# Optimization experiments

Measured on AMD Instinct MI355X. Metric: run time of the kernel, lower is better.

## Reference

```python
import jax, jax.numpy as jnp
import numpy as np

NF, NS, GP = 5, 27, 4


def conv2d(x, w, b):
    y = jax.lax.conv_general_dilated(x, w, (1, 1), 'SAME',
                                     dimension_numbers=('NCHW', 'OIHW', 'NCHW'))
    return y + b[None, :, None, None]


def trilinear_sample(frames, tc, yc, xc):
    # frames: [b, nf, h, w]; tc/yc/xc: [b, NS, h, w] absolute (t, y, x) coords
    b, nf, h, w = frames.shape
    tc = jnp.clip(tc, 0.0, nf - 1.0)
    yc = jnp.clip(yc, 0.0, h - 1.0)
    xc = jnp.clip(xc, 0.0, w - 1.0)
    t0 = jnp.floor(tc); y0 = jnp.floor(yc); x0 = jnp.floor(xc)
    wt = tc - t0; wy = yc - y0; wx = xc - x0
    t0i = t0.astype(jnp.int32); y0i = y0.astype(jnp.int32); x0i = x0.astype(jnp.int32)
    t1i = jnp.minimum(t0i + 1, nf - 1)
    y1i = jnp.minimum(y0i + 1, h - 1)
    x1i = jnp.minimum(x0i + 1, w - 1)
    flat = frames.reshape(b, -1)

    def g(ti, yi, xi):
        idx = (ti * h + yi) * w + xi  # [b, NS, h, w]
        return jnp.take_along_axis(flat, idx.reshape(b, -1), axis=1).reshape(idx.shape)

    c000 = g(t0i, y0i, x0i); c001 = g(t0i, y0i, x1i)
    c010 = g(t0i, y1i, x0i); c011 = g(t0i, y1i, x1i)
    c100 = g(t1i, y0i, x0i); c101 = g(t1i, y0i, x1i)
    c110 = g(t1i, y1i, x0i); c111 = g(t1i, y1i, x1i)
    c00 = c000 * (1 - wx) + c001 * wx
    c01 = c010 * (1 - wx) + c011 * wx
    c10 = c100 * (1 - wx) + c101 * wx
    c11 = c110 * (1 - wx) + c111 * wx
    c0 = c00 * (1 - wy) + c01 * wy
    c1 = c10 * (1 - wy) + c11 * wy
    return c0 * (1 - wt) + c1 * wt


def samp(frames, offset):
    # offset: [b, NS*3, h, w] -> per-sample (dt, dy, dx)
    b, nf, h, w = frames.shape
    off = offset.reshape(b, NS, 3, h, w)
    grid = np.stack(np.meshgrid(np.arange(-1, 2), np.arange(-1, 2), np.arange(-1, 2),
                                indexing='ij'), -1).reshape(NS, 3).astype(np.float32)
    bt = jnp.asarray(grid[:, 0] + (NF - 1) // 2)[None, :, None, None]
    by = jnp.asarray(grid[:, 1])[None, :, None, None]
    bx = jnp.asarray(grid[:, 2])[None, :, None, None]
    yy = jnp.arange(h, dtype=frames.dtype)[None, None, :, None]
    xx = jnp.arange(w, dtype=frames.dtype)[None, None, None, :]
    tc = off[:, :, 0] + bt
    yc = off[:, :, 1] + by + yy
    xc = off[:, :, 2] + bx + xx
    return trilinear_sample(frames, tc, yc, xc)  # [b, NS, h, w]


def reference(frames, ow1, ob1, ow2, ob2, ow3, ob3, ww1, wb1, ww2, wb2, ww3, wb3):
    b, c, h, w = frames.shape
    # OffsetNet: two relu convs -> feat (128 ch), head -> offsets (NS*3 ch)
    f1 = jax.nn.relu(conv2d(frames, ow1, ob1))
    feat = jax.nn.relu(conv2d(f1, ow2, ob2))
    offset = conv2d(feat, ow3, ob3)
    samples = samp(frames, offset)  # [b, 27, h, w]
    cat = jnp.concatenate([frames, feat, samples], axis=1)  # [b, 160, h, w]
    # WeightsNet: three conv+relu
    wgt = jax.nn.relu(conv2d(cat, ww1, wb1))
    wgt = jax.nn.relu(conv2d(wgt, ww2, wb2))
    wgt = jax.nn.relu(conv2d(wgt, ww3, wb3))  # [b, 27, h, w]
    npg = NS // GP  # 6 -> only first GP*npg=24 samples used (torch.split + range(gp))
    s = samples[:, :GP * npg].reshape(b, GP, npg, h, w)
    wg = wgt[:, :GP * npg].reshape(b, GP, npg, h, w)
    gp_pred = GP * jnp.sum(s * wg, axis=2)  # [b, 4, h, w]
    avg = jnp.sum(gp_pred, axis=1, keepdims=True) / NS
    return gp_pred, avg


def setup_inputs() -> dict:
    key = jax.random.key(0)
    ks = jax.random.split(key, 8)
    B, H, W = 4, 512, 512

    def he(k, shape):
        fan_in = shape[1] * shape[2] * shape[3]
        return jax.random.normal(k, shape, jnp.float32) * np.sqrt(2.0 / fan_in)

    return {
        'frames': jax.random.uniform(ks[0], (B, NF, H, W), jnp.float32),
        'ow1': he(ks[1], (64, NF, 3, 3)), 'ob1': jnp.zeros((64,), jnp.float32),
        'ow2': he(ks[2], (128, 64, 3, 3)), 'ob2': jnp.zeros((128,), jnp.float32),
        'ow3': he(ks[3], (NS * 3, 128, 3, 3)) * 0.1, 'ob3': jnp.zeros((NS * 3,), jnp.float32),
        'ww1': he(ks[4], (64, NF + 128 + NS, 3, 3)), 'wb1': jnp.zeros((64,), jnp.float32),
        'ww2': he(ks[5], (64, 64, 3, 3)), 'wb2': jnp.zeros((64,), jnp.float32),
        'ww3': he(ks[6], (NS, 64, 3, 3)), 'wb3': jnp.zeros((NS,), jnp.float32),
    }
```

## Files before the change

### kernel.cpp

```cpp
#include <hip/hip_runtime.h>

#define HH 512
#define WW 512
#define HWP (HH * WW)

typedef unsigned short bf16_t;
typedef short bf16x8 __attribute__((ext_vector_type(8)));
typedef float f32x4 __attribute__((ext_vector_type(4)));
typedef unsigned short us4 __attribute__((ext_vector_type(4)));
typedef unsigned short us8 __attribute__((ext_vector_type(8)));

__device__ __forceinline__ float bf2f(bf16_t h) {
    union { unsigned int u; float f; } v; v.u = ((unsigned int)h) << 16; return v.f;
}
__device__ __forceinline__ bf16_t f2bf(float f) {
    union { float f; unsigned int u; } v; v.f = f;
    unsigned int r = (v.u + 0x7FFFu + ((v.u >> 16) & 1u)) >> 16;
    return (bf16_t)r;
}
__device__ __forceinline__ bf16x8 as_bf(us8 v) {
    union { us8 a; bf16x8 b; } u; u.a = v; return u.b;
}
__device__ __forceinline__ void gload16(const void* g, void* l) {
    __builtin_amdgcn_global_load_lds(
        (const __attribute__((address_space(1))) void*)g,
        (__attribute__((address_space(3))) void*)l, 16, 0, 0);
}

__global__ __launch_bounds__(256) void wprep_all(
    const float* __restrict__ w1, const float* __restrict__ w2,
    const float* __restrict__ w3, const float* __restrict__ w4,
    const float* __restrict__ w5, const float* __restrict__ w6,
    bf16_t* __restrict__ dst)
{
    int i = blockIdx.x * 256 + threadIdx.x;
    if (i >= 350720) return;
    if (i >= 350208) { dst[i] = 0; return; }
    const float* w; int Cout, Cin, COTF, KS, perm, base;
    if (i < 18432)       { w = w1; base = 0;      Cout = 64;  Cin = 5;   COTF = 4; KS = 1; perm = 0; }
    else if (i < 92160)  { w = w2; base = 18432;  Cout = 128; Cin = 64;  COTF = 8; KS = 2; perm = 0; }
    else if (i < 202752) { w = w3; base = 92160;  Cout = 81;  Cin = 128; COTF = 6; KS = 4; perm = 0; }
    else if (i < 294912) { w = w4; base = 202752; Cout = 64;  Cin = 160; COTF = 4; KS = 5; perm = 1; }
    else if (i < 331776) { w = w5; base = 294912; Cout = 64;  Cin = 64;  COTF = 4; KS = 2; perm = 0; }
    else                 { w = w6; base = 331776; Cout = 27;  Cin = 64;  COTF = 2; KS = 2; perm = 0; }
    int r = i - base;
    int j = r & 7;
    int lane = (r >> 3) & 63;
    int cot = (r >> 9) % COTF;
    int rest = r / (512 * COTF);
    int ks = rest % KS, tap = rest / KS;
    int col = lane & 15, hi = lane >> 4;
    int co = cot * 16 + col;
    int ci = ks * 32 + hi * 8 + j;
    float v = 0.f;
    if (co < Cout && ci < Cin) {
        int rci = ci;
        if (perm) rci = (ci < 128) ? ci + 5 : (ci < 133 ? ci - 128 : ci);
        v = w[((size_t)co * Cin + rci) * 9 + tap];
    }
    dst[i] = f2bf(v);
}

template<int COT, int KS, int ZX>
__global__ __launch_bounds__(256, 2) void tconv(
    const bf16_t* __restrict__ in, size_t inImgStride,
    const bf16_t* __restrict__ wt, const float* __restrict__ bias,
    bf16_t* __restrict__ out, size_t outImgStride,
    int COTF, int Cout, int relu, const bf16_t* __restrict__ zp,
    int cinCh, const bf16_t* __restrict__ catp,
    float* __restrict__ fuseOut, int img0)
{
    __shared__ us8 buf[2][1584];
    const int tid = threadIdx.x;
    const int wave = tid >> 6, lane = tid & 63;
    const int col = lane & 15, hi = lane >> 4;
    const int img = blockIdx.y >> 7;
    const int yb0 = (blockIdx.y & 127) * 4;
    const int xb = (ZX ? (blockIdx.x >> 1) : blockIdx.x) * 64;
    const int czbase = (ZX ? (blockIdx.x & 1) : blockIdx.z) * COT;
    const size_t slab = (size_t)HH * WW * 32;

    in += (size_t)img * inImgStride;
    out += (size_t)img * outImgStride;

    int gofs[7];
    bool ok[7];
#pragma unroll
    for (int k = 0; k < 7; ++k) {
        int u = tid + k * 256;
        if (u >= 1584) u = 1583;
        int row = (unsigned)u / 264u;
        int rem = u - row * 264;
        int px = rem >> 2, cs = rem & 3;
        int c = (cs - (px >> 1)) & 3;
        int yin = yb0 - 1 + row;
        int gx = xb - 1 + px;
        ok[k] = ((unsigned)yin < (unsigned)HH) && ((unsigned)gx < (unsigned)WW)
                && (c < cinCh);
        gofs[k] = ok[k] ? (int)(((size_t)yin * WW + gx) * 32 + c * 8) : 0;
    }

    auto STAGE = [&](int nb, int ks) {
#pragma unroll
        for (int k = 0; k < 7; ++k) {
            if (k == 6 && tid >= 48) continue;
            const bf16_t* g = ok[k] ? in + (size_t)ks * slab + gofs[k] : zp;
            gload16(g, (void*)&buf[nb][k * 256 + wave * 64]);
        }
    };

    f32x4 acc[4][COT] = {};
    bf16x8 a[9][COT];

    auto ALOAD = [&](int ks) {
#pragma unroll
        for (int t = 0; t < 9; ++t) {
#pragma unroll
            for (int c = 0; c < COT; ++c)
                a[t][c] = *(const bf16x8*)(wt
                    + (((size_t)t * KS + ks) * COTF + czbase + c) * 512 + lane * 8);
        }
    };

    auto COMPUTE = [&](int cb) {
#pragma unroll
        for (int dx = 0; dx < 3; ++dx) {
            const int X = wave * 16 + col + dx;
            const int ubase = X * 4 + ((hi + (X >> 1)) & 3);
            bf16x8 b[6];
#pragma unroll
            for (int br = 0; br < 6; ++br)
                b[br] = as_bf(buf[cb][br * 264 + ubase]);
#pragma unroll
            for (int dy = 0; dy < 3; ++dy) {
#pragma unroll
                for (int c = 0; c < COT; ++c) {
#pragma unroll
                    for (int r = 0; r < 4; ++r)
                        acc[r][c] = __builtin_amdgcn_mfma_f32_16x16x32_bf16(
                            a[dy * 3 + dx][c], b[r + dy], acc[r][c], 0, 0, 0);
                }
            }
        }
    };

    STAGE(0, 0);
    for (int ks = 0; ks < KS; ++ks) {
        ALOAD(ks);
        __builtin_amdgcn_sched_barrier(0);
        if (ks + 1 < KS) {
            STAGE((ks + 1) & 1, ks + 1);
            __builtin_amdgcn_sched_barrier(0);
            asm volatile("s_waitcnt vmcnt(7)" ::: "memory");
        } else {
            asm volatile("s_waitcnt vmcnt(0)" ::: "memory");
        }
        __builtin_amdgcn_sched_barrier(0);
        __builtin_amdgcn_s_barrier();
        __builtin_amdgcn_sched_barrier(0);
        COMPUTE(ks & 1);
        __builtin_amdgcn_s_barrier();
        __builtin_amdgcn_sched_barrier(0);
    }

    const int x = xb + wave * 16 + col;

    if (fuseOut) {
        int gimg = img0 + img;
        const bf16_t* catim = catp + (size_t)img * inImgStride;
#pragma unroll
        for (int r = 0; r < 4; ++r) {
            int y = yb0 + r;
            const bf16_t* cp = catim + ((size_t)y * WW + x) * 32;
            float p[4] = {0.f, 0.f, 0.f, 0.f};
#pragma unroll
            for (int c = 0; c < COT; ++c) {
                int chb = (czbase + c) * 16 + hi * 4;
#pragma unroll
                for (int j = 0; j < 4; ++j) {
                    int ch = chb + j;
                    if (ch < 24) {
                        float wv = fmaxf(acc[r][c][j] + bias[ch], 0.f);
                        p[ch / 6] += wv * bf2f(cp[5 + ch]);
                    }
                }
            }
#pragma unroll
            for (int g = 0; g < 4; ++g) {
                p[g] += __shfl_xor(p[g], 16);
                p[g] += __shfl_xor(p[g], 32);
            }
            if (hi == 0) {
                size_t pix = (size_t)y * WW + x;
                float tot = 0.f;
#pragma unroll
                for (int g = 0; g < 4; ++g) {
                    float gp = 4.f * p[g];
                    fuseOut[((size_t)gimg * 4 + g) * HWP + pix] = gp;
                    tot += gp;
                }
                fuseOut[(size_t)16 * HWP + (size_t)gimg * HWP + pix] = tot / 27.f;
            }
        }
        return;
    }

#pragma unroll
    for (int c = 0; c < COT; ++c) {
        int chbase = (czbase + c) * 16 + hi * 4;
        int slice = chbase >> 5, rem = chbase & 31;
        float bv[4];
#pragma unroll
        for (int j = 0; j < 4; ++j) {
            int co = chbase + j;
            bv[j] = (co < Cout) ? bias[co] : 0.f;
        }
#pragma unroll
        for (int r = 0; r < 4; ++r) {
            int y = yb0 + r;
            us4 o;
#pragma unroll
            for (int j = 0; j < 4; ++j) {
                float v = acc[r][c][j] + bv[j];
                if (relu) v = fmaxf(v, 0.f);
                o[j] = f2bf(v);
            }
            *(us4*)(out + (((size_t)slice * HH + y) * WW + x) * 32 + rem) = o;
        }
    }
}

__global__ __launch_bounds__(256) void tr_fr32(
    const float* __restrict__ fr0, int img0,
    bf16_t* __restrict__ dst0, size_t stride)
{
    int img = blockIdx.y;
    int i = blockIdx.x * 256 + threadIdx.x;
    const float* fr = fr0 + (size_t)(img0 + img) * 5 * HWP;
    bf16_t* dst = dst0 + (size_t)img * stride;
    us8 v0 = {};
#pragma unroll
    for (int c = 0; c < 5; ++c) v0[c] = f2bf(fr[(size_t)c * HWP + i]);
    *(us8*)(dst + (size_t)i * 32) = v0;
}

__global__ __launch_bounds__(256, 4) void sample27f(
    const float* __restrict__ fr0, int img0,
    const bf16_t* __restrict__ of0, size_t stride,
    bf16_t* __restrict__ cat0)
{
    int img = blockIdx.y;
    int i = blockIdx.x * 256 + threadIdx.x;
    int y = i >> 9, x = i & 511;
    const float* f = fr0 + (size_t)(img0 + img) * 5 * HWP;
    const bf16_t* off = of0 + (size_t)img * stride;
    bf16_t* cat = cat0 + (size_t)img * stride;

    us8 ov[12];
#pragma unroll
    for (int sl = 0; sl < 3; ++sl)
#pragma unroll
        for (int c = 0; c < 4; ++c)
            ov[sl * 4 + c] = *(const us8*)(off
                + (((size_t)sl * HH + y) * WW + x) * 32 + c * 8);

    us8 outv[4];
#pragma unroll
    for (int c = 0; c < 5; ++c)
        outv[0][c] = f2bf(f[(size_t)c * HWP + i]);

#pragma unroll
    for (int s = 0; s < 27; ++s) {
        float dt  = bf2f((bf16_t)ov[(3 * s) >> 3][(3 * s) & 7]);
        float dyo = bf2f((bf16_t)ov[(3 * s + 1) >> 3][(3 * s + 1) & 7]);
        float dxo = bf2f((bf16_t)ov[(3 * s + 2) >> 3][(3 * s + 2) & 7]);
        float tc = dt + (float)(s / 9 + 1);
        float yc = dyo + (float)((s / 3) % 3 - 1) + (float)y;
        float xc = dxo + (float)(s % 3 - 1) + (float)x;
        tc = fminf(fmaxf(tc, 0.f), 4.f);
        yc = fminf(fmaxf(yc, 0.f), 511.f);
        xc = fminf(fmaxf(xc, 0.f), 511.f);
        float t0f = floorf(tc), y0f = floorf(yc), x0f = floorf(xc);
        float wt = tc - t0f, wy = yc - y0f, wx = xc - x0f;
        int t0 = (int)t0f, y0 = (int)y0f, x0 = (int)x0f;
        int t1 = min(t0 + 1, 4), y1 = min(y0 + 1, 511), x1 = min(x0 + 1, 511);
        float c000 = f[((size_t)t0 * HH + y0) * WW + x0];
        float c001 = f[((size_t)t0 * HH + y0) * WW + x1];
        float c010 = f[((size_t)t0 * HH + y1) * WW + x0];
        float c011 = f[((size_t)t0 * HH + y1) * WW + x1];
        float c100 = f[((size_t)t1 * HH + y0) * WW + x0];
        float c101 = f[((size_t)t1 * HH + y0) * WW + x1];
        float c110 = f[((size_t)t1 * HH + y1) * WW + x0];
        float c111 = f[((size_t)t1 * HH + y1) * WW + x1];
        float c00 = c000 * (1.f - wx) + c001 * wx;
        float c01 = c010 * (1.f - wx) + c011 * wx;
        float c10 = c100 * (1.f - wx) + c101 * wx;
        float c11 = c110 * (1.f - wx) + c111 * wx;
        float c0 = c00 * (1.f - wy) + c01 * wy;
        float c1 = c10 * (1.f - wy) + c11 * wy;
        int ch = 5 + s;
        outv[ch >> 3][ch & 7] = f2bf(c0 * (1.f - wt) + c1 * wt);
    }

    us8* o = (us8*)(cat + ((size_t)y * WW + x) * 32);
    o[0] = outv[0]; o[1] = outv[1]; o[2] = outv[2]; o[3] = outv[3];
}

static inline int cdiv(int a, int b) { return (a + b - 1) / b; }

extern "C" void kernel_launch(void* const* d_in, const int* in_sizes, int n_in,
                              void* d_out, int out_size, void* d_ws, size_t ws_size,
                              hipStream_t stream)
{
    const float* frames = (const float*)d_in[0];
    const float* ow1 = (const float*)d_in[1];
    const float* ob1 = (const float*)d_in[2];
    const float* ow2 = (const float*)d_in[3];
    const float* ob2 = (const float*)d_in[4];
    const float* ow3 = (const float*)d_in[5];
    const float* ob3 = (const float*)d_in[6];
    const float* ww1 = (const float*)d_in[7];
    const float* wb1 = (const float*)d_in[8];
    const float* ww2 = (const float*)d_in[9];
    const float* wb2 = (const float*)d_in[10];
    const float* ww3 = (const float*)d_in[11];
    const float* wb3 = (const float*)d_in[12];
    float* out = (float*)d_out;

    bf16_t* Wp = (bf16_t*)d_ws;
    const size_t wo1 = 0;
    const size_t wo2 = 18432;
    const size_t wo3 = 92160;
    const size_t wo4 = 202752;
    const size_t wo5 = 294912;
    const size_t wo6 = 331776;
    const size_t wzp = 350208;
    const size_t wtot = 350720;

    const size_t SLAB = (size_t)HH * WW * 32;
    const size_t PerImg = 7 * SLAB;

    size_t availElems = ws_size / sizeof(bf16_t);
    int NB = 1;
    if (wtot + 4 * PerImg <= availElems) NB = 4;
    else if (wtot + 2 * PerImg <= availElems) NB = 2;

    bf16_t* ZP = Wp + wzp;
    bf16_t* WS = Wp + wtot;

    wprep_all<<<cdiv(350720, 256), 256, 0, stream>>>(ow1, ow2, ow3, ww1, ww2, ww3, Wp);

    for (int s = 0; s < 4; s += NB) {
        int nb = (4 - s < NB) ? (4 - s) : NB;
        bf16_t* S0 = WS;
        bf16_t* S2 = WS + 2 * SLAB;
        bf16_t* S4 = WS + 4 * SLAB;
        bf16_t* S5 = WS + 5 * SLAB;
        bf16_t* S6 = WS + 6 * SLAB;

        tr_fr32<<<dim3(1024, nb), 256, 0, stream>>>(frames, s, S6, PerImg);
        tconv<4, 1, 0><<<dim3(8, 128 * nb, 1), 256, 0, stream>>>(
            S6, PerImg, Wp + wo1, ob1, S4, PerImg, 4, 64, 1, ZP,
            1, nullptr, nullptr, 0);
        tconv<4, 2, 1><<<dim3(16, 128 * nb, 1), 256, 0, stream>>>(
            S4, PerImg, Wp + wo2, ob2, S0, PerImg, 8, 128, 1, ZP,
            4, nullptr, nullptr, 0);
        tconv<3, 4, 1><<<dim3(16, 128 * nb, 1), 256, 0, stream>>>(
            S0, PerImg, Wp + wo3, ob3, S4, PerImg, 6, 81, 0, ZP,
            4, nullptr, nullptr, 0);
        sample27f<<<dim3(1024, nb), 256, 0, stream>>>(frames, s, S4, PerImg, S4);
        tconv<4, 5, 0><<<dim3(8, 128 * nb, 1), 256, 0, stream>>>(
            S0, PerImg, Wp + wo4, wb1, S5, PerImg, 4, 64, 1, ZP,
            4, nullptr, nullptr, 0);
        tconv<4, 2, 0><<<dim3(8, 128 * nb, 1), 256, 0, stream>>>(
            S5, PerImg, Wp + wo5, wb2, S0, PerImg, 4, 64, 1, ZP,
            4, nullptr, nullptr, 0);
        tconv<2, 2, 0><<<dim3(8, 128 * nb, 1), 256, 0, stream>>>(
            S0, PerImg, Wp + wo6, wb3, S2, PerImg, 2, 27, 1, ZP,
            4, S4, out, s);
    }
}
```

Baseline: 1.092 ms.

## Load conv input tiles directly from global memory instead of LDS staging

Removes the LDS double-buffered staging of the input halo tile (global_load_lds plus barriers and waitcnt pipelining) from the tiled conv kernel. Each lane now reads its bf16x8 input fragments straight from global memory, relying on cache, with per-row and per-column validity masks falling back to a zero buffer. This drops shared memory usage and block-level synchronisation, which may raise occupancy, but it loses the explicit overlap of loads with MFMA work and re-reads overlapping halo data across waves through cache.

```diff
diff --git a/kernel.cpp b/kernel.cpp
--- a/kernel.cpp
+++ b/kernel.cpp
@@ -17,14 +17,6 @@
     union { float f; unsigned int u; } v; v.f = f;
     unsigned int r = (v.u + 0x7FFFu + ((v.u >> 16) & 1u)) >> 16;
     return (bf16_t)r;
-}
-__device__ __forceinline__ bf16x8 as_bf(us8 v) {
-    union { us8 a; bf16x8 b; } u; u.a = v; return u.b;
-}
-__device__ __forceinline__ void gload16(const void* g, void* l) {
-    __builtin_amdgcn_global_load_lds(
-        (const __attribute__((address_space(1))) void*)g,
-        (__attribute__((address_space(3))) void*)l, 16, 0, 0);
 }
 
 __global__ __launch_bounds__(256) void wprep_all(
@@ -70,7 +62,6 @@
     int cinCh, const bf16_t* __restrict__ catp,
     float* __restrict__ fuseOut, int img0)
 {
-    __shared__ us8 buf[2][1584];
     const int tid = threadIdx.x;
     const int wave = tid >> 6, lane = tid & 63;
     const int col = lane & 15, hi = lane >> 4;
@@ -83,31 +74,20 @@
     in += (size_t)img * inImgStride;
     out += (size_t)img * outImgStride;
 
-    int gofs[7];
-    bool ok[7];
-#pragma unroll
-    for (int k = 0; k < 7; ++k) {
-        int u = tid + k * 256;
-        if (u >= 1584) u = 1583;
-        int row = (unsigned)u / 264u;
-        int rem = u - row * 264;
-        int px = rem >> 2, cs = rem & 3;
-        int c = (cs - (px >> 1)) & 3;
-        int yin = yb0 - 1 + row;
-        int gx = xb - 1 + px;
-        ok[k] = ((unsigned)yin < (unsigned)HH) && ((unsigned)gx < (unsigned)WW)
-                && (c < cinCh);
-        gofs[k] = ok[k] ? (int)(((size_t)yin * WW + gx) * 32 + c * 8) : 0;
-    }
-
-    auto STAGE = [&](int nb, int ks) {
-#pragma unroll
-        for (int k = 0; k < 7; ++k) {
-            if (k == 6 && tid >= 48) continue;
-            const bf16_t* g = ok[k] ? in + (size_t)ks * slab + gofs[k] : zp;
-            gload16(g, (void*)&buf[nb][k * 256 + wave * 64]);
-        }
-    };
+    int ybase[6]; bool vy[6];
+#pragma unroll
+    for (int br = 0; br < 6; ++br) {
+        int yin = yb0 - 1 + br;
+        vy[br] = (unsigned)yin < (unsigned)HH;
+        ybase[br] = yin * (WW * 32);
+    }
+    int xoff[3]; bool vx[3];
+#pragma unroll
+    for (int dx = 0; dx < 3; ++dx) {
+        int gx = xb - 1 + wave * 16 + col + dx;
+        vx[dx] = ((unsigned)gx < (unsigned)WW) && (hi < cinCh);
+        xoff[dx] = gx * 32 + hi * 8;
+    }
 
     f32x4 acc[4][COT] = {};
     bf16x8 a[9][COT];
@@ -122,15 +102,18 @@
         }
     };
 
-    auto COMPUTE = [&](int cb) {
+    for (int ks = 0; ks < KS; ++ks) {
+        ALOAD(ks);
+        const bf16_t* base = in + (size_t)ks * slab;
 #pragma unroll
         for (int dx = 0; dx < 3; ++dx) {
-            const int X = wave * 16 + col + dx;
-            const int ubase = X * 4 + ((hi + (X >> 1)) & 3);
             bf16x8 b[6];
 #pragma unroll
-            for (int br = 0; br < 6; ++br)
-                b[br] = as_bf(buf[cb][br * 264 + ubase]);
+            for (int br = 0; br < 6; ++br) {
+                const bf16_t* p = (vy[br] && vx[dx])
+                                  ? base + ybase[br] + xoff[dx] : zp;
+                b[br] = *(const bf16x8*)p;
+            }
 #pragma unroll
             for (int dy = 0; dy < 3; ++dy) {
 #pragma unroll
@@ -142,25 +125,6 @@
                 }
             }
         }
-    };
-
-    STAGE(0, 0);
-    for (int ks = 0; ks < KS; ++ks) {
-        ALOAD(ks);
-        __builtin_amdgcn_sched_barrier(0);
-        if (ks + 1 < KS) {
-            STAGE((ks + 1) & 1, ks + 1);
-            __builtin_amdgcn_sched_barrier(0);
-            asm volatile("s_waitcnt vmcnt(7)" ::: "memory");
-        } else {
-            asm volatile("s_waitcnt vmcnt(0)" ::: "memory");
-        }
-        __builtin_amdgcn_sched_barrier(0);
-        __builtin_amdgcn_s_barrier();
-        __builtin_amdgcn_sched_barrier(0);
-        COMPUTE(ks & 1);
-        __builtin_amdgcn_s_barrier();
-        __builtin_amdgcn_sched_barrier(0);
     }
 
     const int x = xb + wave * 16 + col;
```

After: 1.182 ms. 1.08x slower.
